# Optimization experiments

Measured on AMD Instinct MI355X. Metric: run time of the kernel, lower is better.

The kernel has to match this reference:

```python
import jax, jax.numpy as jnp
import numpy as np

D_EV, D_RGB, D_FUSED, D_REASON = 128, 128, 384, 384
D_INNER, D_STATE, D_CONV, DT_RANK = 2 * D_REASON, 16, 4, (D_REASON + 15) // 16
B, L = 4, 1024
LN_EPS = 1e-5


def setup_inputs() -> dict:
    key = jax.random.key(0)
    ks = jax.random.split(key, 16)
    s = lambda k, shp, scale=0.02: jax.random.normal(k, shp, jnp.float32) * scale
    inp = {
        "ev_tok": jax.random.normal(ks[0], (B, L, D_EV), jnp.float32),
        "rgb_tok": jax.random.normal(ks[1], (B, L, D_RGB), jnp.float32),
        "W_ev": s(ks[2], (D_EV, D_FUSED // 2)), "b_ev": jnp.zeros((D_FUSED // 2,), jnp.float32),
        "W_rgb": s(ks[3], (D_RGB, D_FUSED // 2)), "b_rgb": jnp.zeros((D_FUSED // 2,), jnp.float32),
        "ln_g": jnp.ones((D_FUSED,), jnp.float32), "ln_b": jnp.zeros((D_FUSED,), jnp.float32),
        "W_proj": s(ks[4], (D_FUSED, D_REASON)), "b_proj": jnp.zeros((D_REASON,), jnp.float32),
        "W_in": s(ks[5], (D_REASON, 2 * D_INNER)),
        "conv_w": s(ks[6], (D_INNER, 1, D_CONV), 0.1), "conv_b": jnp.zeros((D_INNER,), jnp.float32),
        "W_x": s(ks[7], (D_INNER, DT_RANK + 2 * D_STATE)),
        "W_dt": s(ks[8], (DT_RANK, D_INNER), 0.1), "b_dt": s(ks[9], (D_INNER,), 0.1),
        "A_log": jnp.tile(jnp.log(jnp.arange(1, D_STATE + 1, dtype=jnp.float32)), (D_INNER, 1)),
        "D_skip": jnp.ones((D_INNER,), jnp.float32),
        "W_out": s(ks[10], (D_INNER, D_REASON)),
    }
    return inp


def _selective_scan(u, delta, A, Bm, Cm, D_skip):
    # u, delta: [B,L,d]; Bm, Cm: [B,L,n]; A: [d,n]; D_skip: [d]
    deltaA = jnp.exp(delta[..., None] * A)                       # [B,L,d,n]
    deltaBu = delta[..., None] * Bm[:, :, None, :] * u[..., None]  # [B,L,d,n]

    def step(h, inp):
        dA, dBu, C_t = inp
        h = dA * h + dBu                                         # [B,d,n]
        y = jnp.einsum('bdn,bn->bd', h, C_t)
        return h, y

    h0 = jnp.zeros((u.shape[0], A.shape[0], A.shape[1]), u.dtype)
    xs = (jnp.moveaxis(deltaA, 1, 0), jnp.moveaxis(deltaBu, 1, 0), jnp.moveaxis(Cm, 1, 0))
    _, ys = jax.lax.scan(step, h0, xs)                           # [L,B,d]
    return jnp.moveaxis(ys, 0, 1) + u * D_skip


def _mamba_block(x, W_in, conv_w, conv_b, W_x, W_dt, b_dt, A_log, D_skip, W_out):
    xr = x @ W_in                                                # [B,L,2*d_inner]
    u, res = jnp.split(xr, 2, axis=-1)
    # causal depthwise conv over time
    uc = jnp.swapaxes(u, 1, 2)                                   # [B,d_inner,L]
    uc = jax.lax.conv_general_dilated(uc, conv_w, (1,), [(D_CONV - 1, 0)],
                                      dimension_numbers=('NCH', 'OIH', 'NCH'),
                                      feature_group_count=D_INNER)
    u = jax.nn.silu(jnp.swapaxes(uc, 1, 2) + conv_b)             # [B,L,d_inner]
    x_dbl = u @ W_x                                              # [B,L,dt_rank+2n]
    dt, Bm, Cm = jnp.split(x_dbl, [DT_RANK, DT_RANK + D_STATE], axis=-1)
    delta = jax.nn.softplus(dt @ W_dt + b_dt)                    # [B,L,d_inner]
    A = -jnp.exp(A_log)                                          # [d_inner,n]
    y = _selective_scan(u, delta, A, Bm, Cm, D_skip)
    y = y * jax.nn.silu(res)
    return y @ W_out


def reference(ev_tok, rgb_tok, W_ev, b_ev, W_rgb, b_rgb, ln_g, ln_b, W_proj, b_proj,
              W_in, conv_w, conv_b, W_x, W_dt, b_dt, A_log, D_skip, W_out):
    x = jnp.concatenate([ev_tok @ W_ev + b_ev, rgb_tok @ W_rgb + b_rgb], axis=-1)
    mu = jnp.mean(x, axis=-1, keepdims=True)
    var = jnp.mean(jnp.square(x - mu), axis=-1, keepdims=True)
    x = (x - mu) * jax.lax.rsqrt(var + LN_EPS) * ln_g + ln_b
    x = x @ W_proj + b_proj                                      # [B,L,d_reason]
    return _mamba_block(x, W_in, conv_w, conv_b, W_x, W_dt, b_dt, A_log, D_skip, W_out)
```

## Files before the change

kernel.cpp:

```cpp
#include <hip/hip_runtime.h>
#include <cstddef>
#include <cstdint>

#define L_SEQ 1024
#define NCHUNK 64
#define CLEN 16

typedef __bf16 bf16x8 __attribute__((ext_vector_type(8)));
typedef float f32x4 __attribute__((ext_vector_type(4)));

__device__ __forceinline__ float silu_f(float x) {
    return x / (1.f + __expf(-x));
}

__device__ __forceinline__ float exp2_fast(float x) {
    return exp2f(x);
}

__device__ __forceinline__ unsigned short f2bf(float x) {
    union { float f; unsigned int u; } v; v.f = x;
    unsigned int r = (v.u + 0x7fffu + ((v.u >> 16) & 1u)) >> 16;
    return (unsigned short)r;
}
__device__ __forceinline__ float bf2f(unsigned short h) {
    union { float f; unsigned int u; } v; v.u = ((unsigned int)h) << 16;
    return v.f;
}
__device__ __forceinline__ unsigned int packf(float x) {
    unsigned short h = f2bf(x);
    unsigned short l = f2bf(x - bf2f(h));
    return ((unsigned int)h << 16) | (unsigned int)l;
}
__device__ __forceinline__ float unpackf(unsigned int pk) {
    return bf2f((unsigned short)(pk >> 16)) + bf2f((unsigned short)(pk & 0xffffu));
}

__global__ __launch_bounds__(256)
void gemm64(const float* __restrict__ A, int lda,
            const float* __restrict__ B, int ldb,
            float* __restrict__ Cf, int ldc,
            int M, int N, int K)
{
    __shared__ float As[16][68];
    __shared__ float Bs[16][64];
    const int tid = threadIdx.x;
    const int tx = tid & 15, ty = tid >> 4;
    const int m0 = blockIdx.y * 64, n0 = blockIdx.x * 64;
    const int arow = tid >> 2, acol = (tid & 3) << 2;
    const int brow = tid >> 4, bcol = (tid & 15) << 2;
    float acc[4][4] = {};
    const float* Ap = A + (size_t)(m0 + arow) * lda + acol;
    const float* Bp = B + (size_t)brow * ldb + n0 + bcol;
    const bool bok = (n0 + bcol) < N;
    for (int k0 = 0; k0 < K; k0 += 16) {
        float4 av = make_float4(0.f, 0.f, 0.f, 0.f);
        float4 bv = make_float4(0.f, 0.f, 0.f, 0.f);
        if (k0 + acol < K) av = *(const float4*)(Ap + k0);
        if (bok && (k0 + brow) < K) bv = *(const float4*)(Bp + (size_t)k0 * ldb);
        As[acol + 0][arow] = av.x;
        As[acol + 1][arow] = av.y;
        As[acol + 2][arow] = av.z;
        As[acol + 3][arow] = av.w;
        *(float4*)&Bs[brow][bcol] = bv;
        __syncthreads();
        #pragma unroll
        for (int k = 0; k < 16; ++k) {
            float4 a4 = *(const float4*)&As[k][ty * 4];
            float4 b4 = *(const float4*)&Bs[k][tx * 4];
            float aa[4] = {a4.x, a4.y, a4.z, a4.w};
            float bb[4] = {b4.x, b4.y, b4.z, b4.w};
            #pragma unroll
            for (int i = 0; i < 4; ++i)
                #pragma unroll
                for (int j = 0; j < 4; ++j)
                    acc[i][j] = fmaf(aa[i], bb[j], acc[i][j]);
        }
        __syncthreads();
    }
    const int nn = n0 + tx * 4;
    if (nn >= N) return;
    #pragma unroll
    for (int i = 0; i < 4; ++i) {
        int m = m0 + ty * 4 + i;
        *(float4*)(Cf + (size_t)m * ldc + nn) =
            make_float4(acc[i][0], acc[i][1], acc[i][2], acc[i][3]);
    }
}

template<bool APK, int EPI>
__global__ __launch_bounds__(256)
void gemm_bf3(const unsigned short* __restrict__ Ahi,
              const unsigned short* __restrict__ Alo,
              const unsigned int* __restrict__ Apk, int lda,
              const unsigned short* __restrict__ Bthi,
              const unsigned short* __restrict__ Btlo,
              const float* __restrict__ bias,
              float* __restrict__ Cf, float* __restrict__ Cf2,
              unsigned short* __restrict__ Chi, unsigned short* __restrict__ Clo,
              int ldc, int K)
{
    __shared__ unsigned short As[2][128][40];
    __shared__ unsigned short Bs[2][128][40];
    const int tid = threadIdx.x;
    const int lane = tid & 63;
    const int wave = tid >> 6;
    const int wm = wave >> 1, wn = wave & 1;
    const int m0 = blockIdx.y * 128, n0 = blockIdx.x * 128;
    const int srow = tid >> 1, sko = (tid & 1) * 16;

    f32x4 acc[4][4];
    #pragma unroll
    for (int i = 0; i < 4; ++i)
        #pragma unroll
        for (int j = 0; j < 4; ++j) {
            f32x4 z = {0.f, 0.f, 0.f, 0.f};
            acc[i][j] = z;
        }

    const size_t aoff = (size_t)(m0 + srow) * lda + sko;
    const size_t boff = (size_t)(n0 + srow) * K + sko;

    for (int k0 = 0; k0 < K; k0 += 32) {
        if constexpr (!APK) {
            uint4 h0 = *(const uint4*)(Ahi + aoff + k0);
            uint4 h1 = *(const uint4*)(Ahi + aoff + k0 + 8);
            uint4 l0 = *(const uint4*)(Alo + aoff + k0);
            uint4 l1 = *(const uint4*)(Alo + aoff + k0 + 8);
            *(uint4*)&As[0][srow][sko]     = h0;
            *(uint4*)&As[0][srow][sko + 8] = h1;
            *(uint4*)&As[1][srow][sko]     = l0;
            *(uint4*)&As[1][srow][sko + 8] = l1;
        } else {
            const unsigned int* ap = Apk + aoff + k0;
            uint4 p0 = *(const uint4*)(ap);
            uint4 p1 = *(const uint4*)(ap + 4);
            uint4 p2 = *(const uint4*)(ap + 8);
            uint4 p3 = *(const uint4*)(ap + 12);
            uint4 h0, h1, l0, l1;
            h0.x = (p0.x >> 16) | (p0.y & 0xffff0000u);
            h0.y = (p0.z >> 16) | (p0.w & 0xffff0000u);
            h0.z = (p1.x >> 16) | (p1.y & 0xffff0000u);
            h0.w = (p1.z >> 16) | (p1.w & 0xffff0000u);
            h1.x = (p2.x >> 16) | (p2.y & 0xffff0000u);
            h1.y = (p2.z >> 16) | (p2.w & 0xffff0000u);
            h1.z = (p3.x >> 16) | (p3.y & 0xffff0000u);
            h1.w = (p3.z >> 16) | (p3.w & 0xffff0000u);
            l0.x = (p0.x & 0xffffu) | (p0.y << 16);
            l0.y = (p0.z & 0xffffu) | (p0.w << 16);
            l0.z = (p1.x & 0xffffu) | (p1.y << 16);
            l0.w = (p1.z & 0xffffu) | (p1.w << 16);
            l1.x = (p2.x & 0xffffu) | (p2.y << 16);
            l1.y = (p2.z & 0xffffu) | (p2.w << 16);
            l1.z = (p3.x & 0xffffu) | (p3.y << 16);
            l1.w = (p3.z & 0xffffu) | (p3.w << 16);
            *(uint4*)&As[0][srow][sko]     = h0;
            *(uint4*)&As[0][srow][sko + 8] = h1;
            *(uint4*)&As[1][srow][sko]     = l0;
            *(uint4*)&As[1][srow][sko + 8] = l1;
        }
        {
            uint4 bh0 = *(const uint4*)(Bthi + boff + k0);
            uint4 bh1 = *(const uint4*)(Bthi + boff + k0 + 8);
            uint4 bl0 = *(const uint4*)(Btlo + boff + k0);
            uint4 bl1 = *(const uint4*)(Btlo + boff + k0 + 8);
            *(uint4*)&Bs[0][srow][sko]     = bh0;
            *(uint4*)&Bs[0][srow][sko + 8] = bh1;
            *(uint4*)&Bs[1][srow][sko]     = bl0;
            *(uint4*)&Bs[1][srow][sko + 8] = bl1;
        }
        __syncthreads();
        const int fr = lane & 15, kq = lane >> 4;
        bf16x8 aH[4], aL[4];
        #pragma unroll
        for (int i = 0; i < 4; ++i) {
            aH[i] = *(const bf16x8*)&As[0][wm * 64 + i * 16 + fr][kq * 8];
            aL[i] = *(const bf16x8*)&As[1][wm * 64 + i * 16 + fr][kq * 8];
        }
        #pragma unroll
        for (int j = 0; j < 4; ++j) {
            bf16x8 bH = *(const bf16x8*)&Bs[0][wn * 64 + j * 16 + fr][kq * 8];
            bf16x8 bL = *(const bf16x8*)&Bs[1][wn * 64 + j * 16 + fr][kq * 8];
            #pragma unroll
            for (int i = 0; i < 4; ++i)
                acc[i][j] = __builtin_amdgcn_mfma_f32_16x16x32_bf16(aH[i], bH, acc[i][j], 0, 0, 0);
            #pragma unroll
            for (int i = 0; i < 4; ++i)
                acc[i][j] = __builtin_amdgcn_mfma_f32_16x16x32_bf16(aL[i], bH, acc[i][j], 0, 0, 0);
            #pragma unroll
            for (int i = 0; i < 4; ++i)
                acc[i][j] = __builtin_amdgcn_mfma_f32_16x16x32_bf16(aH[i], bL, acc[i][j], 0, 0, 0);
        }
        __syncthreads();
    }
    const int col = lane & 15, rq = lane >> 4;
    #pragma unroll
    for (int j = 0; j < 4; ++j) {
        int nn = n0 + wn * 64 + j * 16 + col;
        float bv = 0.f;
        if constexpr (EPI == 0 || EPI == 1) { if (bias) bv = bias[nn]; }
        if constexpr (EPI == 2) { if (nn >= 32 && nn < 800) bv = bias[nn - 32]; }
        #pragma unroll
        for (int i = 0; i < 4; ++i) {
            int mb = m0 + wm * 64 + i * 16 + rq * 4;
            #pragma unroll
            for (int r = 0; r < 4; ++r) {
                float o = acc[i][j][r] + bv;
                if constexpr (EPI == 0) {
                    Cf[(size_t)(mb + r) * ldc + nn] = o;
                } else if constexpr (EPI == 1) {
                    unsigned short h = f2bf(o);
                    Chi[(size_t)(mb + r) * ldc + nn] = h;
                    Clo[(size_t)(mb + r) * ldc + nn] = f2bf(o - bf2f(h));
                } else {
                    if (nn < 32) {
                        Cf2[(size_t)(mb + r) * 32 + nn] = o;
                    } else if (nn < 800) {
                        float sp = fmaxf(o, 0.f) + log1pf(expf(-fabsf(o)));
                        Cf[(size_t)(mb + r) * ldc + (nn - 32)] = sp;
                    }
                }
            }
        }
    }
}

__global__ __launch_bounds__(256)
void wcvt(const float* __restrict__ W, unsigned short* __restrict__ Thi,
          unsigned short* __restrict__ Tlo, int K, int N)
{
    __shared__ float t[32][33];
    const int tid = threadIdx.x;
    const int n0 = blockIdx.x * 32, k0 = blockIdx.y * 32;
    const int r = tid >> 3, c4 = (tid & 7) * 4;
    float4 v = *(const float4*)(W + (size_t)(k0 + r) * N + n0 + c4);
    t[r][c4 + 0] = v.x; t[r][c4 + 1] = v.y; t[r][c4 + 2] = v.z; t[r][c4 + 3] = v.w;
    __syncthreads();
    unsigned short hs[4], ls[4];
    #pragma unroll
    for (int j = 0; j < 4; ++j) {
        float x = t[c4 + j][r];
        hs[j] = f2bf(x);
        ls[j] = f2bf(x - bf2f(hs[j]));
    }
    size_t o = (size_t)(n0 + r) * K + k0 + c4;
    uint2 hv, lv;
    hv.x = (unsigned)hs[0] | ((unsigned)hs[1] << 16);
    hv.y = (unsigned)hs[2] | ((unsigned)hs[3] << 16);
    lv.x = (unsigned)ls[0] | ((unsigned)ls[1] << 16);
    lv.y = (unsigned)ls[2] | ((unsigned)ls[3] << 16);
    *(uint2*)(Thi + o) = hv;
    *(uint2*)(Tlo + o) = lv;
}

__global__ __launch_bounds__(256)
void pad_btc(const float* __restrict__ W_x,
             unsigned short* __restrict__ Thi, unsigned short* __restrict__ Tlo)
{
    const int flat = blockIdx.x * 256 + threadIdx.x;
    const int r = flat / 768, k = flat % 768;
    const int row = (r < 32) ? r : (768 + r);
    float val = (r < 32) ? W_x[(size_t)k * 56 + 24 + r] : 0.f;
    unsigned short h = f2bf(val);
    Thi[(size_t)row * 768 + k] = h;
    Tlo[(size_t)row * 768 + k] = f2bf(val - bf2f(h));
}

__global__ __launch_bounds__(256)
void embed_pack(const float* __restrict__ ev, const float* __restrict__ rgb,
                unsigned int* __restrict__ apk)
{
    const int m = blockIdx.x, kk = threadIdx.x;
    float val = (kk < 128) ? ev[(size_t)m * 128 + kk] : rgb[(size_t)m * 128 + kk - 128];
    apk[(size_t)m * 256 + kk] = packf(val);
}

__global__ __launch_bounds__(256)
void wcat_cvt(const float* __restrict__ W_ev, const float* __restrict__ W_rgb,
              const float* __restrict__ b_ev, const float* __restrict__ b_rgb,
              unsigned short* __restrict__ Thi, unsigned short* __restrict__ Tlo,
              float* __restrict__ biascat)
{
    const int flat = blockIdx.x * 256 + threadIdx.x;
    if (flat < 384 * 256) {
        const int n = flat >> 8, k = flat & 255;
        float val = 0.f;
        if (n < 192) { if (k < 128) val = W_ev[(size_t)k * 192 + n]; }
        else         { if (k >= 128) val = W_rgb[(size_t)(k - 128) * 192 + (n - 192)]; }
        unsigned short h = f2bf(val);
        Thi[flat] = h;
        Tlo[flat] = f2bf(val - bf2f(h));
    } else if (flat < 384 * 256 + 384) {
        const int i = flat - 384 * 256;
        biascat[i] = (i < 192) ? b_ev[i] : b_rgb[i - 192];
    }
}

__global__ __launch_bounds__(256)
void ln2(unsigned short* __restrict__ hi, unsigned short* __restrict__ lo,
         const float* __restrict__ g, const float* __restrict__ b)
{
    const int lane = threadIdx.x & 63;
    const int row = blockIdx.x * 4 + (threadIdx.x >> 6);
    unsigned short* ph = hi + (size_t)row * 384;
    unsigned short* pl = lo + (size_t)row * 384;
    float v[6];
    #pragma unroll
    for (int i = 0; i < 6; ++i) {
        int c = i * 64 + lane;
        v[i] = bf2f(ph[c]) + bf2f(pl[c]);
    }
    float s = v[0] + v[1] + v[2] + v[3] + v[4] + v[5];
    #pragma unroll
    for (int m = 32; m >= 1; m >>= 1) s += __shfl_xor(s, m);
    const float mu = s * (1.f / 384.f);
    float q = 0.f;
    #pragma unroll
    for (int i = 0; i < 6; ++i) { float dv = v[i] - mu; q = fmaf(dv, dv, q); }
    #pragma unroll
    for (int m = 32; m >= 1; m >>= 1) q += __shfl_xor(q, m);
    const float inv = 1.f / sqrtf(q * (1.f / 384.f) + 1e-5f);
    #pragma unroll
    for (int i = 0; i < 6; ++i) {
        int c = i * 64 + lane;
        float o = (v[i] - mu) * inv * g[c] + b[c];
        unsigned short h = f2bf(o);
        ph[c] = h;
        pl[c] = f2bf(o - bf2f(h));
    }
}

__global__ __launch_bounds__(256)
void conv_pack(const float* __restrict__ xr, const float* __restrict__ conv_w,
               const float* __restrict__ conv_b, unsigned int* __restrict__ upk)
{
    const int d = blockIdx.x * 256 + threadIdx.x;
    const int t0 = blockIdx.z * L_SEQ + blockIdx.y * 16;
    const float w0 = conv_w[d * 4 + 0], w1 = conv_w[d * 4 + 1];
    const float w2 = conv_w[d * 4 + 2], w3 = conv_w[d * 4 + 3];
    const float cb = conv_b[d];
    const float* xp = xr + (size_t)t0 * 1536 + d;
    float x1, x2, x3;
    if (blockIdx.y == 0) { x1 = x2 = x3 = 0.f; }
    else {
        x1 = xp[-1 * 1536];
        x2 = xp[-2 * 1536];
        x3 = xp[-3 * 1536];
    }
    unsigned int* op = upk + (size_t)t0 * 768 + d;
    #pragma unroll 4
    for (int i = 0; i < 16; ++i) {
        float cur = xp[i * 1536];
        float a = cb;
        a = fmaf(x3, w0, a);
        a = fmaf(x2, w1, a);
        a = fmaf(x1, w2, a);
        a = fmaf(cur, w3, a);
        op[i * 768] = packf(silu_f(a));
        x3 = x2; x2 = x1; x1 = cur;
    }
}

__global__ __launch_bounds__(256)
void scan_a2(const float* __restrict__ delta, const unsigned int* __restrict__ upk,
             const float* __restrict__ bc, const float* __restrict__ A_log,
             float* __restrict__ dsum_out, float* __restrict__ Bc)
{
    __shared__ float Bsh[CLEN][16];
    const int tid = threadIdx.x;
    const int d = blockIdx.x * 256 + tid;
    const int c = blockIdx.y, b = blockIdx.z;
    const int row0 = b * L_SEQ + c * CLEN;
    {
        int t = tid >> 4, n = tid & 15;
        Bsh[t][n] = bc[(size_t)(row0 + t) * 32 + n];
    }
    float AL2[16];
    {
        const float* ap = A_log + d * 16;
        #pragma unroll
        for (int n = 0; n < 16; ++n)
            AL2[n] = -__expf(ap[n]) * 1.44269504f;
    }
    __syncthreads();
    float h[16];
    #pragma unroll
    for (int n = 0; n < 16; ++n) h[n] = 0.f;
    float dsum = 0.f;
    const float* dp = delta + (size_t)row0 * 768 + d;
    const unsigned int* up = upk + (size_t)row0 * 768 + d;
    #pragma unroll 4
    for (int t = 0; t < CLEN; ++t) {
        float dt = dp[t * 768];
        float ut = unpackf(up[t * 768]);
        float du = dt * ut;
        dsum += dt;
        #pragma unroll
        for (int n = 0; n < 16; ++n) {
            float dA = exp2_fast(dt * AL2[n]);
            h[n] = fmaf(dA, h[n], du * Bsh[t][n]);
        }
    }
    dsum_out[(size_t)(b * 768 + d) * NCHUNK + c] = dsum;
    float* bcp = Bc + (((size_t)(b * 768 + d)) * NCHUNK + c) * 16;
    #pragma unroll
    for (int n = 0; n < 16; ++n) bcp[n] = h[n];
}

__global__ __launch_bounds__(256)
void scan_b2(const float* __restrict__ dsum, const float* __restrict__ A_log,
             float* __restrict__ BcHin)
{
    const size_t flat = (size_t)blockIdx.x * 256 + threadIdx.x;
    const size_t bd = flat >> 4;
    const int n = (int)(flat & 15);
    const int d = (int)(bd % 768);
    const float AL2 = -__expf(A_log[d * 16 + n]) * 1.44269504f;
    const float* dsp = dsum + bd * NCHUNK;
    const size_t base = bd * (NCHUNK * 16) + n;
    float h = 0.f;
    for (int c = 0; c < NCHUNK; ++c) {
        size_t i = base + (size_t)c * 16;
        float a = exp2_fast(AL2 * dsp[c]);
        float bb = BcHin[i];
        BcHin[i] = h;
        h = fmaf(a, h, bb);
    }
}

__global__ __launch_bounds__(256)
void scan_c2(float* __restrict__ delta, const unsigned int* __restrict__ upk,
             const float* __restrict__ bc, const float* __restrict__ A_log,
             const float* __restrict__ Hin, const float* __restrict__ D_skip,
             const float* __restrict__ xr)
{
    __shared__ float Bsh[CLEN][16];
    __shared__ float Csh[CLEN][16];
    const int tid = threadIdx.x;
    const int d = blockIdx.x * 256 + tid;
    const int c = blockIdx.y, b = blockIdx.z;
    const int row0 = b * L_SEQ + c * CLEN;
    {
        int t = tid >> 4, n = tid & 15;
        const float* xp = bc + (size_t)(row0 + t) * 32;
        Bsh[t][n] = xp[n];
        Csh[t][n] = xp[16 + n];
    }
    float AL2[16];
    {
        const float* ap = A_log + d * 16;
        #pragma unroll
        for (int n = 0; n < 16; ++n)
            AL2[n] = -__expf(ap[n]) * 1.44269504f;
    }
    float h[16];
    {
        const float* hp = Hin + (((size_t)(b * 768 + d)) * NCHUNK + c) * 16;
        #pragma unroll
        for (int n = 0; n < 16; ++n) h[n] = hp[n];
    }
    const float Ds = D_skip[d];
    __syncthreads();
    float* dp = delta + (size_t)row0 * 768 + d;
    const unsigned int* up = upk + (size_t)row0 * 768 + d;
    const float* rp = xr + (size_t)row0 * 1536 + 768 + d;
    #pragma unroll 4
    for (int t = 0; t < CLEN; ++t) {
        float dt = dp[t * 768];
        float ut = unpackf(up[t * 768]);
        float du = dt * ut;
        float y = 0.f;
        #pragma unroll
        for (int n = 0; n < 16; ++n) {
            float dA = exp2_fast(dt * AL2[n]);
            h[n] = fmaf(dA, h[n], du * Bsh[t][n]);
            y = fmaf(h[n], Csh[t][n], y);
        }
        float res = rp[t * 1536];
        float gy = fmaf(ut, Ds, y) * silu_f(res);
        dp[t * 768] = __builtin_bit_cast(float, packf(gy));
    }
}

extern "C" void kernel_launch(void* const* d_in, const int* in_sizes, int n_in,
                              void* d_out, int out_size, void* d_ws, size_t ws_size,
                              hipStream_t stream)
{
    const float* ev     = (const float*)d_in[0];
    const float* rgb    = (const float*)d_in[1];
    const float* W_ev   = (const float*)d_in[2];
    const float* b_ev   = (const float*)d_in[3];
    const float* W_rgb  = (const float*)d_in[4];
    const float* b_rgb  = (const float*)d_in[5];
    const float* ln_g   = (const float*)d_in[6];
    const float* ln_b   = (const float*)d_in[7];
    const float* W_proj = (const float*)d_in[8];
    const float* b_proj = (const float*)d_in[9];
    const float* W_in   = (const float*)d_in[10];
    const float* conv_w = (const float*)d_in[11];
    const float* conv_b = (const float*)d_in[12];
    const float* W_x    = (const float*)d_in[13];
    const float* W_dt   = (const float*)d_in[14];
    const float* b_dt   = (const float*)d_in[15];
    const float* A_log  = (const float*)d_in[16];
    const float* D_skip = (const float*)d_in[17];
    const float* W_out  = (const float*)d_in[18];
    float* out = (float*)d_out;

    float* ws = (float*)d_ws;
    unsigned short* xfh  = (unsigned short*)ws;
    unsigned short* xfl  = xfh + 1572864;
    float* dsum          = ws;
    float* bc            = ws + 196608;
    unsigned short* xmmh = (unsigned short*)(ws + 1572864);
    unsigned short* xmml = xmmh + 1572864;
    unsigned int* upk    = (unsigned int*)(ws + 1572864);
    float* xr            = ws + 4718592;
    unsigned int* apk    = (unsigned int*)xr;
    float* delta         = ws + 11239424;
    float* BcHin         = ws + 14385152;
    unsigned short* wtp_hi = (unsigned short*)BcHin;
    unsigned short* wtp_lo = wtp_hi + 147456;
    unsigned short* wti_hi = wtp_lo + 147456;
    unsigned short* wti_lo = wti_hi + 589824;
    float* Wcf             = BcHin + 737280;
    unsigned short* btc_hi = (unsigned short*)(BcHin + 1327104);
    unsigned short* btc_lo = btc_hi + 688128;
    unsigned short* wct_hi = (unsigned short*)(BcHin + 2015232);
    unsigned short* wct_lo = wct_hi + 98304;
    float* biascat         = BcHin + 2113536;
    unsigned short* wto_hi = (unsigned short*)(ws + 17530880);
    unsigned short* wto_lo = wto_hi + 294912;

    dim3 blk(256);

    wcvt<<<dim3(12, 12), blk, 0, stream>>>(W_proj, wtp_hi, wtp_lo, 384, 384);
    wcvt<<<dim3(48, 12), blk, 0, stream>>>(W_in,   wti_hi, wti_lo, 384, 1536);
    wcvt<<<dim3(12, 24), blk, 0, stream>>>(W_out,  wto_hi, wto_lo, 768, 384);
    gemm64<<<dim3(12, 12), blk, 0, stream>>>(W_x, 56, W_dt, 768, Wcf, 768, 768, 768, 24);
    pad_btc<<<384, blk, 0, stream>>>(W_x, btc_hi, btc_lo);
    wcvt<<<dim3(24, 24), blk, 0, stream>>>(Wcf, btc_hi + 32 * 768, btc_lo + 32 * 768, 768, 768);
    embed_pack<<<4096, blk, 0, stream>>>(ev, rgb, apk);
    wcat_cvt<<<386, blk, 0, stream>>>(W_ev, W_rgb, b_ev, b_rgb, wct_hi, wct_lo, biascat);

    gemm_bf3<true, 1><<<dim3(3, 32), blk, 0, stream>>>(
        nullptr, nullptr, apk, 256, wct_hi, wct_lo, biascat,
        nullptr, nullptr, xfh, xfl, 384, 256);
    ln2<<<1024, blk, 0, stream>>>(xfh, xfl, ln_g, ln_b);
    gemm_bf3<false, 1><<<dim3(3, 32), blk, 0, stream>>>(
        xfh, xfl, nullptr, 384, wtp_hi, wtp_lo, b_proj,
        nullptr, nullptr, xmmh, xmml, 384, 384);
    gemm_bf3<false, 0><<<dim3(12, 32), blk, 0, stream>>>(
        xmmh, xmml, nullptr, 384, wti_hi, wti_lo, nullptr,
        xr, nullptr, nullptr, nullptr, 1536, 384);
    conv_pack<<<dim3(3, 64, 4), blk, 0, stream>>>(xr, conv_w, conv_b, upk);
    gemm_bf3<true, 2><<<dim3(7, 32), blk, 0, stream>>>(
        nullptr, nullptr, upk, 768, btc_hi, btc_lo, b_dt,
        delta, bc, nullptr, nullptr, 768, 768);
    scan_a2<<<dim3(3, NCHUNK, 4), blk, 0, stream>>>(delta, upk, bc, A_log, dsum, BcHin);
    scan_b2<<<192, blk, 0, stream>>>(dsum, A_log, BcHin);
    scan_c2<<<dim3(3, NCHUNK, 4), blk, 0, stream>>>(delta, upk, bc, A_log, BcHin, D_skip, xr);
    gemm_bf3<true, 0><<<dim3(3, 32), blk, 0, stream>>>(
        nullptr, nullptr, (const unsigned int*)delta, 768, wto_hi, wto_lo, nullptr,
        out, nullptr, nullptr, nullptr, 384, 768);
}
```

Measured before the change: 262.6 us.

## Merge weight-prep kernels into one launch and double-buffer GEMM LDS tiles

Eight separate weight conversion and input packing kernels, including the small gemm64 for W_x·W_dt, become one prep_all kernel that dispatches on block index. The fused W_x·W_dt product is computed directly in transposed bf16 hi/lo form, which removes the intermediate Wcf buffer. The bf16x3 GEMM now uses double-buffered shared memory with register prefetch of the next K tile, plus an 8-way block-index swizzle. Together these cut launch overhead and overlap global loads with MFMA work, at the cost of doubled LDS per block (lower occupancy) and a direct dot product in prep that reads W_dt with strided, uncoalesced loads.

```diff
diff --git a/kernel.cpp b/kernel.cpp
--- a/kernel.cpp
+++ b/kernel.cpp
@@ -33,58 +33,6 @@
 }
 __device__ __forceinline__ float unpackf(unsigned int pk) {
     return bf2f((unsigned short)(pk >> 16)) + bf2f((unsigned short)(pk & 0xffffu));
-}
-
-__global__ __launch_bounds__(256)
-void gemm64(const float* __restrict__ A, int lda,
-            const float* __restrict__ B, int ldb,
-            float* __restrict__ Cf, int ldc,
-            int M, int N, int K)
-{
-    __shared__ float As[16][68];
-    __shared__ float Bs[16][64];
-    const int tid = threadIdx.x;
-    const int tx = tid & 15, ty = tid >> 4;
-    const int m0 = blockIdx.y * 64, n0 = blockIdx.x * 64;
-    const int arow = tid >> 2, acol = (tid & 3) << 2;
-    const int brow = tid >> 4, bcol = (tid & 15) << 2;
-    float acc[4][4] = {};
-    const float* Ap = A + (size_t)(m0 + arow) * lda + acol;
-    const float* Bp = B + (size_t)brow * ldb + n0 + bcol;
-    const bool bok = (n0 + bcol) < N;
-    for (int k0 = 0; k0 < K; k0 += 16) {
-        float4 av = make_float4(0.f, 0.f, 0.f, 0.f);
-        float4 bv = make_float4(0.f, 0.f, 0.f, 0.f);
-        if (k0 + acol < K) av = *(const float4*)(Ap + k0);
-        if (bok && (k0 + brow) < K) bv = *(const float4*)(Bp + (size_t)k0 * ldb);
-        As[acol + 0][arow] = av.x;
-        As[acol + 1][arow] = av.y;
-        As[acol + 2][arow] = av.z;
-        As[acol + 3][arow] = av.w;
-        *(float4*)&Bs[brow][bcol] = bv;
-        __syncthreads();
-        #pragma unroll
-        for (int k = 0; k < 16; ++k) {
-            float4 a4 = *(const float4*)&As[k][ty * 4];
-            float4 b4 = *(const float4*)&Bs[k][tx * 4];
-            float aa[4] = {a4.x, a4.y, a4.z, a4.w};
-            float bb[4] = {b4.x, b4.y, b4.z, b4.w};
-            #pragma unroll
-            for (int i = 0; i < 4; ++i)
-                #pragma unroll
-                for (int j = 0; j < 4; ++j)
-                    acc[i][j] = fmaf(aa[i], bb[j], acc[i][j]);
-        }
-        __syncthreads();
-    }
-    const int nn = n0 + tx * 4;
-    if (nn >= N) return;
-    #pragma unroll
-    for (int i = 0; i < 4; ++i) {
-        int m = m0 + ty * 4 + i;
-        *(float4*)(Cf + (size_t)m * ldc + nn) =
-            make_float4(acc[i][0], acc[i][1], acc[i][2], acc[i][3]);
-    }
 }
 
 template<bool APK, int EPI>
@@ -99,13 +47,20 @@
               unsigned short* __restrict__ Chi, unsigned short* __restrict__ Clo,
               int ldc, int K)
 {
-    __shared__ unsigned short As[2][128][40];
-    __shared__ unsigned short Bs[2][128][40];
+    __shared__ unsigned short As[2][2][128][40];
+    __shared__ unsigned short Bs[2][2][128][40];
     const int tid = threadIdx.x;
     const int lane = tid & 63;
     const int wave = tid >> 6;
     const int wm = wave >> 1, wn = wave & 1;
-    const int m0 = blockIdx.y * 128, n0 = blockIdx.x * 128;
+
+    const int gx = gridDim.x;
+    const int nwg = gx * gridDim.y;
+    const int lin = blockIdx.y * gx + blockIdx.x;
+    const int chunk = nwg >> 3;
+    const int swz = (lin & 7) * chunk + (lin >> 3);
+    const int m0 = (swz / gx) * 128, n0 = (swz % gx) * 128;
+
     const int srow = tid >> 1, sko = (tid & 1) * 16;
 
     f32x4 acc[4][4];
@@ -120,23 +75,31 @@
     const size_t aoff = (size_t)(m0 + srow) * lda + sko;
     const size_t boff = (size_t)(n0 + srow) * K + sko;
 
-    for (int k0 = 0; k0 < K; k0 += 32) {
-        if constexpr (!APK) {
-            uint4 h0 = *(const uint4*)(Ahi + aoff + k0);
-            uint4 h1 = *(const uint4*)(Ahi + aoff + k0 + 8);
-            uint4 l0 = *(const uint4*)(Alo + aoff + k0);
-            uint4 l1 = *(const uint4*)(Alo + aoff + k0 + 8);
-            *(uint4*)&As[0][srow][sko]     = h0;
-            *(uint4*)&As[0][srow][sko + 8] = h1;
-            *(uint4*)&As[1][srow][sko]     = l0;
-            *(uint4*)&As[1][srow][sko + 8] = l1;
+    uint4 ra[4], rb[4];
+
+    auto load_regs = [&](int k0) {
+        if constexpr (APK) {
+            const unsigned int* ap = Apk + aoff + k0;
+            ra[0] = *(const uint4*)(ap);
+            ra[1] = *(const uint4*)(ap + 4);
+            ra[2] = *(const uint4*)(ap + 8);
+            ra[3] = *(const uint4*)(ap + 12);
         } else {
-            const unsigned int* ap = Apk + aoff + k0;
-            uint4 p0 = *(const uint4*)(ap);
-            uint4 p1 = *(const uint4*)(ap + 4);
-            uint4 p2 = *(const uint4*)(ap + 8);
-            uint4 p3 = *(const uint4*)(ap + 12);
-            uint4 h0, h1, l0, l1;
+            ra[0] = *(const uint4*)(Ahi + aoff + k0);
+            ra[1] = *(const uint4*)(Ahi + aoff + k0 + 8);
+            ra[2] = *(const uint4*)(Alo + aoff + k0);
+            ra[3] = *(const uint4*)(Alo + aoff + k0 + 8);
+        }
+        rb[0] = *(const uint4*)(Bthi + boff + k0);
+        rb[1] = *(const uint4*)(Bthi + boff + k0 + 8);
+        rb[2] = *(const uint4*)(Btlo + boff + k0);
+        rb[3] = *(const uint4*)(Btlo + boff + k0 + 8);
+    };
+
+    auto store_lds = [&](int buf) {
+        uint4 h0, h1, l0, l1;
+        if constexpr (APK) {
+            uint4 p0 = ra[0], p1 = ra[1], p2 = ra[2], p3 = ra[3];
             h0.x = (p0.x >> 16) | (p0.y & 0xffff0000u);
             h0.y = (p0.z >> 16) | (p0.w & 0xffff0000u);
             h0.z = (p1.x >> 16) | (p1.y & 0xffff0000u);
@@ -153,45 +116,57 @@
             l1.y = (p2.z & 0xffffu) | (p2.w << 16);
             l1.z = (p3.x & 0xffffu) | (p3.y << 16);
             l1.w = (p3.z & 0xffffu) | (p3.w << 16);
-            *(uint4*)&As[0][srow][sko]     = h0;
-            *(uint4*)&As[0][srow][sko + 8] = h1;
-            *(uint4*)&As[1][srow][sko]     = l0;
-            *(uint4*)&As[1][srow][sko + 8] = l1;
-        }
+        } else {
+            h0 = ra[0]; h1 = ra[1]; l0 = ra[2]; l1 = ra[3];
+        }
+        *(uint4*)&As[buf][0][srow][sko]     = h0;
+        *(uint4*)&As[buf][0][srow][sko + 8] = h1;
+        *(uint4*)&As[buf][1][srow][sko]     = l0;
+        *(uint4*)&As[buf][1][srow][sko + 8] = l1;
+        *(uint4*)&Bs[buf][0][srow][sko]     = rb[0];
+        *(uint4*)&Bs[buf][0][srow][sko + 8] = rb[1];
+        *(uint4*)&Bs[buf][1][srow][sko]     = rb[2];
+        *(uint4*)&Bs[buf][1][srow][sko + 8] = rb[3];
+    };
+
+    const int fr = lane & 15, kq = lane >> 4;
+
+    load_regs(0);
+    store_lds(0);
+    __syncthreads();
+
+    int cur = 0;
+    for (int k0 = 32; ; k0 += 32) {
+        const bool more = k0 < K;
+        if (more) load_regs(k0);
         {
-            uint4 bh0 = *(const uint4*)(Bthi + boff + k0);
-            uint4 bh1 = *(const uint4*)(Bthi + boff + k0 + 8);
-            uint4 bl0 = *(const uint4*)(Btlo + boff + k0);
-            uint4 bl1 = *(const uint4*)(Btlo + boff + k0 + 8);
-            *(uint4*)&Bs[0][srow][sko]     = bh0;
-            *(uint4*)&Bs[0][srow][sko + 8] = bh1;
-            *(uint4*)&Bs[1][srow][sko]     = bl0;
-            *(uint4*)&Bs[1][srow][sko + 8] = bl1;
-        }
+            bf16x8 aH[4], aL[4];
+            #pragma unroll
+            for (int i = 0; i < 4; ++i) {
+                aH[i] = *(const bf16x8*)&As[cur][0][wm * 64 + i * 16 + fr][kq * 8];
+                aL[i] = *(const bf16x8*)&As[cur][1][wm * 64 + i * 16 + fr][kq * 8];
+            }
+            #pragma unroll
+            for (int j = 0; j < 4; ++j) {
+                bf16x8 bH = *(const bf16x8*)&Bs[cur][0][wn * 64 + j * 16 + fr][kq * 8];
+                bf16x8 bL = *(const bf16x8*)&Bs[cur][1][wn * 64 + j * 16 + fr][kq * 8];
+                #pragma unroll
+                for (int i = 0; i < 4; ++i)
+                    acc[i][j] = __builtin_amdgcn_mfma_f32_16x16x32_bf16(aH[i], bH, acc[i][j], 0, 0, 0);
+                #pragma unroll
+                for (int i = 0; i < 4; ++i)
+                    acc[i][j] = __builtin_amdgcn_mfma_f32_16x16x32_bf16(aL[i], bH, acc[i][j], 0, 0, 0);
+                #pragma unroll
+                for (int i = 0; i < 4; ++i)
+                    acc[i][j] = __builtin_amdgcn_mfma_f32_16x16x32_bf16(aH[i], bL, acc[i][j], 0, 0, 0);
+            }
+        }
+        if (!more) break;
+        store_lds(cur ^ 1);
         __syncthreads();
-        const int fr = lane & 15, kq = lane >> 4;
-        bf16x8 aH[4], aL[4];
-        #pragma unroll
-        for (int i = 0; i < 4; ++i) {
-            aH[i] = *(const bf16x8*)&As[0][wm * 64 + i * 16 + fr][kq * 8];
-            aL[i] = *(const bf16x8*)&As[1][wm * 64 + i * 16 + fr][kq * 8];
-        }
-        #pragma unroll
-        for (int j = 0; j < 4; ++j) {
-            bf16x8 bH = *(const bf16x8*)&Bs[0][wn * 64 + j * 16 + fr][kq * 8];
-            bf16x8 bL = *(const bf16x8*)&Bs[1][wn * 64 + j * 16 + fr][kq * 8];
-            #pragma unroll
-            for (int i = 0; i < 4; ++i)
-                acc[i][j] = __builtin_amdgcn_mfma_f32_16x16x32_bf16(aH[i], bH, acc[i][j], 0, 0, 0);
-            #pragma unroll
-            for (int i = 0; i < 4; ++i)
-                acc[i][j] = __builtin_amdgcn_mfma_f32_16x16x32_bf16(aL[i], bH, acc[i][j], 0, 0, 0);
-            #pragma unroll
-            for (int i = 0; i < 4; ++i)
-                acc[i][j] = __builtin_amdgcn_mfma_f32_16x16x32_bf16(aH[i], bL, acc[i][j], 0, 0, 0);
-        }
-        __syncthreads();
-    }
+        cur ^= 1;
+    }
+
     const int col = lane & 15, rq = lane >> 4;
     #pragma unroll
     for (int j = 0; j < 4; ++j) {
@@ -224,21 +199,22 @@
     }
 }
 
-__global__ __launch_bounds__(256)
-void wcvt(const float* __restrict__ W, unsigned short* __restrict__ Thi,
-          unsigned short* __restrict__ Tlo, int K, int N)
-{
-    __shared__ float t[32][33];
-    const int tid = threadIdx.x;
-    const int n0 = blockIdx.x * 32, k0 = blockIdx.y * 32;
+__device__ __forceinline__ void wcvt_body(const float* __restrict__ W,
+                                          unsigned short* __restrict__ Thi,
+                                          unsigned short* __restrict__ Tlo,
+                                          int K, int N, int nx, int local, int tid,
+                                          float* t )
+{
+    const int n0 = (local % nx) * 32, k0 = (local / nx) * 32;
     const int r = tid >> 3, c4 = (tid & 7) * 4;
     float4 v = *(const float4*)(W + (size_t)(k0 + r) * N + n0 + c4);
-    t[r][c4 + 0] = v.x; t[r][c4 + 1] = v.y; t[r][c4 + 2] = v.z; t[r][c4 + 3] = v.w;
+    t[r * 33 + c4 + 0] = v.x; t[r * 33 + c4 + 1] = v.y;
+    t[r * 33 + c4 + 2] = v.z; t[r * 33 + c4 + 3] = v.w;
     __syncthreads();
     unsigned short hs[4], ls[4];
     #pragma unroll
     for (int j = 0; j < 4; ++j) {
-        float x = t[c4 + j][r];
+        float x = t[(c4 + j) * 33 + r];
         hs[j] = f2bf(x);
         ls[j] = f2bf(x - bf2f(hs[j]));
     }
@@ -253,45 +229,70 @@
 }
 
 __global__ __launch_bounds__(256)
-void pad_btc(const float* __restrict__ W_x,
-             unsigned short* __restrict__ Thi, unsigned short* __restrict__ Tlo)
-{
-    const int flat = blockIdx.x * 256 + threadIdx.x;
-    const int r = flat / 768, k = flat % 768;
-    const int row = (r < 32) ? r : (768 + r);
-    float val = (r < 32) ? W_x[(size_t)k * 56 + 24 + r] : 0.f;
-    unsigned short h = f2bf(val);
-    Thi[(size_t)row * 768 + k] = h;
-    Tlo[(size_t)row * 768 + k] = f2bf(val - bf2f(h));
-}
-
-__global__ __launch_bounds__(256)
-void embed_pack(const float* __restrict__ ev, const float* __restrict__ rgb,
-                unsigned int* __restrict__ apk)
-{
-    const int m = blockIdx.x, kk = threadIdx.x;
-    float val = (kk < 128) ? ev[(size_t)m * 128 + kk] : rgb[(size_t)m * 128 + kk - 128];
-    apk[(size_t)m * 256 + kk] = packf(val);
-}
-
-__global__ __launch_bounds__(256)
-void wcat_cvt(const float* __restrict__ W_ev, const float* __restrict__ W_rgb,
+void prep_all(const float* __restrict__ W_proj, const float* __restrict__ W_in,
+              const float* __restrict__ W_out, const float* __restrict__ W_x,
+              const float* __restrict__ W_dt,
+              const float* __restrict__ W_ev, const float* __restrict__ W_rgb,
               const float* __restrict__ b_ev, const float* __restrict__ b_rgb,
-              unsigned short* __restrict__ Thi, unsigned short* __restrict__ Tlo,
-              float* __restrict__ biascat)
-{
-    const int flat = blockIdx.x * 256 + threadIdx.x;
-    if (flat < 384 * 256) {
-        const int n = flat >> 8, k = flat & 255;
-        float val = 0.f;
-        if (n < 192) { if (k < 128) val = W_ev[(size_t)k * 192 + n]; }
-        else         { if (k >= 128) val = W_rgb[(size_t)(k - 128) * 192 + (n - 192)]; }
+              const float* __restrict__ ev, const float* __restrict__ rgb,
+              unsigned short* __restrict__ wtp_hi, unsigned short* __restrict__ wtp_lo,
+              unsigned short* __restrict__ wti_hi, unsigned short* __restrict__ wti_lo,
+              unsigned short* __restrict__ wto_hi, unsigned short* __restrict__ wto_lo,
+              unsigned short* __restrict__ btc_hi, unsigned short* __restrict__ btc_lo,
+              unsigned short* __restrict__ wct_hi, unsigned short* __restrict__ wct_lo,
+              float* __restrict__ biascat, unsigned int* __restrict__ apk)
+{
+    __shared__ float t[32 * 33];
+    const int blk = blockIdx.x;
+    const int tid = threadIdx.x;
+    if (blk < 144) {
+        wcvt_body(W_proj, wtp_hi, wtp_lo, 384, 384, 12, blk, tid, t);
+    } else if (blk < 720) {
+        wcvt_body(W_in, wti_hi, wti_lo, 384, 1536, 48, blk - 144, tid, t);
+    } else if (blk < 1008) {
+        wcvt_body(W_out, wto_hi, wto_lo, 768, 384, 12, blk - 720, tid, t);
+    } else if (blk < 1392) {
+        const int flat = (blk - 1008) * 256 + tid;
+        const int r = flat / 768, k = flat % 768;
+        const int row = (r < 32) ? r : (768 + r);
+        float val = (r < 32) ? W_x[(size_t)k * 56 + 24 + r] : 0.f;
         unsigned short h = f2bf(val);
-        Thi[flat] = h;
-        Tlo[flat] = f2bf(val - bf2f(h));
-    } else if (flat < 384 * 256 + 384) {
-        const int i = flat - 384 * 256;
-        biascat[i] = (i < 192) ? b_ev[i] : b_rgb[i - 192];
+        btc_hi[(size_t)row * 768 + k] = h;
+        btc_lo[(size_t)row * 768 + k] = f2bf(val - bf2f(h));
+    } else if (blk < 3696) {
+        const int flat = (blk - 1392) * 256 + tid;
+        const int j = flat / 768, k = flat % 768;
+        const float* xp = W_x + (size_t)k * 56;
+        float acc = 0.f;
+        #pragma unroll
+        for (int r = 0; r < 24; ++r)
+            acc = fmaf(xp[r], W_dt[(size_t)r * 768 + j], acc);
+        unsigned short h = f2bf(acc);
+        btc_hi[(size_t)(32 + j) * 768 + k] = h;
+        btc_lo[(size_t)(32 + j) * 768 + k] = f2bf(acc - bf2f(h));
+    } else if (blk < 4082) {
+        const int flat = (blk - 3696) * 256 + tid;
+        if (flat < 384 * 256) {
+            const int n = flat >> 8, k = flat & 255;
+            float val = 0.f;
+            if (n < 192) { if (k < 128) val = W_ev[(size_t)k * 192 + n]; }
+            else         { if (k >= 128) val = W_rgb[(size_t)(k - 128) * 192 + (n - 192)]; }
+            unsigned short h = f2bf(val);
+            wct_hi[flat] = h;
+            wct_lo[flat] = f2bf(val - bf2f(h));
+        } else if (flat < 384 * 256 + 384) {
+            const int i = flat - 384 * 256;
+            biascat[i] = (i < 192) ? b_ev[i] : b_rgb[i - 192];
+        }
+    } else {
+        const int idx = (blk - 4082) * 1024 + tid * 4;
+        const int m = idx >> 8, kk = idx & 255;
+        #pragma unroll
+        for (int q = 0; q < 4; ++q) {
+            int k = kk + q;
+            float val = (k < 128) ? ev[(size_t)m * 128 + k] : rgb[(size_t)m * 128 + k - 128];
+            apk[(size_t)m * 256 + k] = packf(val);
+        }
     }
 }
 
@@ -522,25 +523,20 @@
     unsigned short* wtp_lo = wtp_hi + 147456;
     unsigned short* wti_hi = wtp_lo + 147456;
     unsigned short* wti_lo = wti_hi + 589824;
-    float* Wcf             = BcHin + 737280;
-    unsigned short* btc_hi = (unsigned short*)(BcHin + 1327104);
+    unsigned short* btc_hi = (unsigned short*)(BcHin + 737280);
     unsigned short* btc_lo = btc_hi + 688128;
-    unsigned short* wct_hi = (unsigned short*)(BcHin + 2015232);
+    unsigned short* wct_hi = (unsigned short*)(BcHin + 1425408);
     unsigned short* wct_lo = wct_hi + 98304;
-    float* biascat         = BcHin + 2113536;
+    float* biascat         = BcHin + 1523712;
     unsigned short* wto_hi = (unsigned short*)(ws + 17530880);
     unsigned short* wto_lo = wto_hi + 294912;
 
     dim3 blk(256);
 
-    wcvt<<<dim3(12, 12), blk, 0, stream>>>(W_proj, wtp_hi, wtp_lo, 384, 384);
-    wcvt<<<dim3(48, 12), blk, 0, stream>>>(W_in,   wti_hi, wti_lo, 384, 1536);
-    wcvt<<<dim3(12, 24), blk, 0, stream>>>(W_out,  wto_hi, wto_lo, 768, 384);
-    gemm64<<<dim3(12, 12), blk, 0, stream>>>(W_x, 56, W_dt, 768, Wcf, 768, 768, 768, 24);
-    pad_btc<<<384, blk, 0, stream>>>(W_x, btc_hi, btc_lo);
-    wcvt<<<dim3(24, 24), blk, 0, stream>>>(Wcf, btc_hi + 32 * 768, btc_lo + 32 * 768, 768, 768);
-    embed_pack<<<4096, blk, 0, stream>>>(ev, rgb, apk);
-    wcat_cvt<<<386, blk, 0, stream>>>(W_ev, W_rgb, b_ev, b_rgb, wct_hi, wct_lo, biascat);
+    prep_all<<<5106, blk, 0, stream>>>(
+        W_proj, W_in, W_out, W_x, W_dt, W_ev, W_rgb, b_ev, b_rgb, ev, rgb,
+        wtp_hi, wtp_lo, wti_hi, wti_lo, wto_hi, wto_lo,
+        btc_hi, btc_lo, wct_hi, wct_lo, biascat, apk);
 
     gemm_bf3<true, 1><<<dim3(3, 32), blk, 0, stream>>>(
         nullptr, nullptr, apk, 256, wct_hi, wct_lo, biascat,
```

Measured after the change: 282.7 us. +7.6%, slower.
